# Kernel optimization log

Hardware: AMD Instinct MI355X
Metric: run time of the kernel (lower is better)

The kernel has to match this reference:

```python
import jax, jax.numpy as jnp
import numpy as np


def setup_inputs() -> dict:
    key = jax.random.key(0)
    kq, kk, kv = jax.random.split(key, 3)
    B, S, D = 8, 2048, 128
    Q = jax.random.normal(kq, (B, S, D), dtype=jnp.float32)
    K = jax.random.normal(kk, (B, S, D), dtype=jnp.float32)
    V = jax.random.normal(kv, (B, S, D), dtype=jnp.float32)
    return {"Q": Q, "K": K, "V": V}


def reference(Q, K, V):
    # scores: [B, S, S]
    d = Q.shape[-1]
    scores = jnp.einsum('bqd,bkd->bqk', Q, K) / jnp.sqrt(jnp.float32(d))
    # causal mask: position i attends to keys <= i (original sets upper triangle to -inf)
    S = scores.shape[-1]
    causal = jnp.tril(jnp.ones((S, S), dtype=bool))  # [S, S]
    scores = jnp.where(causal[None, :, :], scores, -jnp.inf)
    probs = jax.nn.softmax(scores, axis=-1)
    return jnp.einsum('bqk,bkd->bqd', probs, V)
```

## Files before the change

### kernel.cpp

```cpp
#include <hip/hip_runtime.h>

#define BB 8
#define SS 2048
#define DD 128

typedef _Float16 f16;
typedef _Float16 f16x8 __attribute__((ext_vector_type(8)));
typedef float f32x4 __attribute__((ext_vector_type(4)));

#define SWV(d) ((((d) & 7) ^ (((d) >> 3) & 7)) << 3)

static __device__ __forceinline__ unsigned short f2h(float x) {
    f16 h = (f16)x;
    return __builtin_bit_cast(unsigned short, h);
}

static __device__ __forceinline__ float fast_exp2(float x) {
#if __has_builtin(__builtin_amdgcn_exp2f)
    return __builtin_amdgcn_exp2f(x);
#else
    return exp2f(x);
#endif
}

template <int NS>
__global__ __launch_bounds__(256, 2)
void attn_fwd(const float* __restrict__ Qg, const float* __restrict__ Kg,
              const float* __restrict__ Vg, float* __restrict__ Og,
              float* __restrict__ Opart, float2* __restrict__ mlb)
{
    __shared__ __align__(16) f16 Kl[64 * 128];
    __shared__ __align__(16) f16 Vt[128 * 64];
    __shared__ __align__(16) f16 Pl[4][16 * 64];

    const int tid  = threadIdx.x;
    const int lane = tid & 63;
    const int w    = tid >> 6;
    const int c_   = lane & 15;
    const int g    = lane >> 4;

    const int L   = blockIdx.x;
    const int bb  = L & 7;
    const int rem = L >> 3;
    const int qb  = 31 - (rem / NS);
    const int s   = rem % NS;
    const int T   = qb + 1;
    const int t0  = (T * s) / NS;
    const int t1  = (T * (s + 1)) / NS;

    const int qrow0 = qb * 64 + w * 16;

    const float qs = 0.08838834764831845f * 1.4426950408889634f;
    f16x8 qf[4];
    {
        const float* qp = Qg + (size_t)(bb * SS + qrow0 + c_) * DD;
#pragma unroll
        for (int kk = 0; kk < 4; ++kk) {
            const int d0 = kk * 32 + g * 8;
            f32x4 a = *(const f32x4*)(qp + d0);
            f32x4 b = *(const f32x4*)(qp + d0 + 4);
            f16x8 q;
#pragma unroll
            for (int i = 0; i < 4; ++i) {
                q[i]     = (f16)(a[i] * qs);
                q[i + 4] = (f16)(b[i] * qs);
            }
            qf[kk] = q;
        }
    }

    f32x4 Oa[8];
#pragma unroll
    for (int i = 0; i < 8; ++i) Oa[i] = (f32x4){0.f, 0.f, 0.f, 0.f};
    float mrun[4] = {-1e30f, -1e30f, -1e30f, -1e30f};
    float lpart[4] = {0.f, 0.f, 0.f, 0.f};

    f16* Pw = &Pl[w][0];

    const int krow = tid >> 5;
    const int kc4  = tid & 31;
    const int vkg  = tid >> 5;
    const int vq   = tid & 31;

    f32x4 kreg[8], vreg[8];

    if (t0 < t1) {
        {
            const size_t gb = (size_t)(bb * SS + t0 * 64) * DD;
#pragma unroll
            for (int j = 0; j < 8; ++j)
                kreg[j] = *(const f32x4*)(Kg + gb + (krow + 8 * j) * DD + kc4 * 4);
#pragma unroll
            for (int i = 0; i < 8; ++i)
                vreg[i] = *(const f32x4*)(Vg + gb + (vkg * 8 + i) * DD + vq * 4);
        }

        for (int t = t0; t < t1; ++t) {
            __syncthreads();
#pragma unroll
            for (int j = 0; j < 8; ++j) {
                const int row = krow + 8 * j;
                const int el  = row * 128 + ((kc4 * 4) ^ ((row & 7) << 3));
                f32x4 v = kreg[j];
                ushort4 u;
                u.x = f2h(v[0]); u.y = f2h(v[1]); u.z = f2h(v[2]); u.w = f2h(v[3]);
                *(ushort4*)&Kl[el] = u;
            }
#pragma unroll
            for (int dd = 0; dd < 4; ++dd) {
                const int d  = vq * 4 + dd;
                const int sw = SWV(d);
#pragma unroll
                for (int h = 0; h < 2; ++h) {
                    ushort4 u;
                    u.x = f2h(vreg[4 * h + 0][dd]);
                    u.y = f2h(vreg[4 * h + 1][dd]);
                    u.z = f2h(vreg[4 * h + 2][dd]);
                    u.w = f2h(vreg[4 * h + 3][dd]);
                    const int el = d * 64 + ((vkg * 8 + 4 * h) ^ sw);
                    *(ushort4*)&Vt[el] = u;
                }
            }
            __syncthreads();

            if (t + 1 < t1) {
                const size_t gb = (size_t)(bb * SS + (t + 1) * 64) * DD;
#pragma unroll
                for (int j = 0; j < 8; ++j)
                    kreg[j] = *(const f32x4*)(Kg + gb + (krow + 8 * j) * DD + kc4 * 4);
#pragma unroll
                for (int i = 0; i < 8; ++i)
                    vreg[i] = *(const f32x4*)(Vg + gb + (vkg * 8 + i) * DD + vq * 4);
            }

            const int kbase = t * 64;

            f32x4 s4[4];
            __builtin_amdgcn_s_setprio(1);
#pragma unroll
            for (int nb = 0; nb < 4; ++nb) {
                f32x4 acc = (f32x4){0.f, 0.f, 0.f, 0.f};
                const int row = c_ + nb * 16;
                const int sw  = (row & 7) << 3;
#pragma unroll
                for (int kk = 0; kk < 4; ++kk) {
                    f16x8 kb = *(const f16x8*)&Kl[row * 128 + ((kk * 32 + g * 8) ^ sw)];
                    acc = __builtin_amdgcn_mfma_f32_16x16x32_f16(qf[kk], kb, acc, 0, 0, 0);
                }
                s4[nb] = acc;
            }
            __builtin_amdgcn_s_setprio(0);

            if (t == qb) {
#pragma unroll
                for (int nb = 0; nb < 4; ++nb)
#pragma unroll
                    for (int r = 0; r < 4; ++r) {
                        const int kj = kbase + nb * 16 + c_;
                        const int qi = qrow0 + g * 4 + r;
                        if (kj > qi) s4[nb][r] = -1e30f;
                    }
            }

            float pm[4], sc[4];
#pragma unroll
            for (int r = 0; r < 4; ++r) {
                float v = fmaxf(fmaxf(s4[0][r], s4[1][r]), fmaxf(s4[2][r], s4[3][r]));
                v = fmaxf(v, __shfl_xor(v, 1));
                v = fmaxf(v, __shfl_xor(v, 2));
                v = fmaxf(v, __shfl_xor(v, 4));
                v = fmaxf(v, __shfl_xor(v, 8));
                pm[r] = v;
            }
#pragma unroll
            for (int r = 0; r < 4; ++r) {
                const bool keep = (pm[r] - mrun[r] <= 8.0f);
                const float mn  = keep ? mrun[r] : pm[r];
                sc[r]   = keep ? 1.0f : fast_exp2(mrun[r] - pm[r]);
                mrun[r] = mn;
            }
            float rs[4] = {0.f, 0.f, 0.f, 0.f};
            f16 pv16[4][4];
#pragma unroll
            for (int nb = 0; nb < 4; ++nb)
#pragma unroll
                for (int r = 0; r < 4; ++r) {
                    float pv = fast_exp2(s4[nb][r] - mrun[r]);
                    rs[r] += pv;
                    pv16[nb][r] = (f16)pv;
                }
            const float scmin = fminf(fminf(sc[0], sc[1]), fminf(sc[2], sc[3]));
            if (scmin < 1.0f) {
#pragma unroll
                for (int dblk = 0; dblk < 8; ++dblk)
#pragma unroll
                    for (int r = 0; r < 4; ++r) Oa[dblk][r] *= sc[r];
            }
#pragma unroll
            for (int r = 0; r < 4; ++r) lpart[r] = lpart[r] * sc[r] + rs[r];

#pragma unroll
            for (int nb = 0; nb < 4; ++nb)
#pragma unroll
                for (int r = 0; r < 4; ++r) {
                    const int row = g * 4 + r;
                    Pw[row * 64 + ((nb * 16 + c_) ^ ((row & 7) << 3))] = pv16[nb][r];
                }

#pragma unroll
            for (int ks = 0; ks < 2; ++ks) {
                f16x8 pa = *(const f16x8*)&Pw[c_ * 64 + ((ks * 32 + g * 8) ^ ((c_ & 7) << 3))];
                __builtin_amdgcn_s_setprio(1);
#pragma unroll
                for (int dblk = 0; dblk < 8; ++dblk) {
                    const int d  = dblk * 16 + c_;
                    f16x8 vb = *(const f16x8*)&Vt[d * 64 + ((ks * 32 + g * 8) ^ SWV(d))];
                    Oa[dblk] = __builtin_amdgcn_mfma_f32_16x16x32_f16(pa, vb, Oa[dblk], 0, 0, 0);
                }
                __builtin_amdgcn_s_setprio(0);
            }
        }
    }

    float lrun[4];
#pragma unroll
    for (int r = 0; r < 4; ++r) {
        float v = lpart[r];
        v += __shfl_xor(v, 1);
        v += __shfl_xor(v, 2);
        v += __shfl_xor(v, 4);
        v += __shfl_xor(v, 8);
        lrun[r] = v;
    }

    if (NS == 1) {
#pragma unroll
        for (int r = 0; r < 4; ++r) {
            const int qrow = qrow0 + g * 4 + r;
            float* dst = Og + (size_t)(bb * SS + qrow) * DD + c_;
            const float inv = 1.0f / lrun[r];
#pragma unroll
            for (int dblk = 0; dblk < 8; ++dblk) dst[dblk * 16] = Oa[dblk][r] * inv;
        }
    } else {
        float*  od  = (s == 0) ? Og : (Opart + (size_t)(s - 1) * BB * SS * DD);
        float2* mld = mlb + (size_t)s * BB * SS;
#pragma unroll
        for (int r = 0; r < 4; ++r) {
            const int qrow = qrow0 + g * 4 + r;
            float* dst = od + (size_t)(bb * SS + qrow) * DD + c_;
#pragma unroll
            for (int dblk = 0; dblk < 8; ++dblk) dst[dblk * 16] = Oa[dblk][r];
            if (c_ == 0) mld[bb * SS + qrow] = make_float2(mrun[r], lrun[r]);
        }
    }
}

template <int NS>
__global__ __launch_bounds__(256)
void merge_kernel(float* __restrict__ out, const float* __restrict__ Opart,
                  const float2* __restrict__ mlb)
{
    const int idx = blockIdx.x * 256 + threadIdx.x;
    const int row = idx >> 5;
    float2 ml[NS];
#pragma unroll
    for (int i = 0; i < NS; ++i) ml[i] = mlb[(size_t)i * BB * SS + row];
    float mm = ml[0].x;
#pragma unroll
    for (int i = 1; i < NS; ++i) mm = fmaxf(mm, ml[i].x);
    float e[NS], den = 0.f;
#pragma unroll
    for (int i = 0; i < NS; ++i) {
        e[i] = fast_exp2(ml[i].x - mm);
        den += ml[i].y * e[i];
    }
    const float inv = 1.0f / den;
    float4 o = ((const float4*)out)[idx];
    float4 acc;
    acc.x = o.x * e[0]; acc.y = o.y * e[0];
    acc.z = o.z * e[0]; acc.w = o.w * e[0];
#pragma unroll
    for (int i = 1; i < NS; ++i) {
        float4 p = ((const float4*)(Opart + (size_t)(i - 1) * BB * SS * DD))[idx];
        acc.x += p.x * e[i]; acc.y += p.y * e[i];
        acc.z += p.z * e[i]; acc.w += p.w * e[i];
    }
    acc.x *= inv; acc.y *= inv; acc.z *= inv; acc.w *= inv;
    ((float4*)out)[idx] = acc;
}

extern "C" void kernel_launch(void* const* d_in, const int* in_sizes, int n_in,
                              void* d_out, int out_size, void* d_ws, size_t ws_size,
                              hipStream_t stream)
{
    const float* Q = (const float*)d_in[0];
    const float* K = (const float*)d_in[1];
    const float* V = (const float*)d_in[2];
    float* out = (float*)d_out;

    const size_t OB = (size_t)BB * SS * DD * sizeof(float);
    const size_t MB_ = (size_t)BB * SS * sizeof(float2);
    const int mergeGrid = BB * SS * DD / 4 / 256;

    const size_t need4 = 3 * OB + 4 * MB_;
    const size_t need2 = 1 * OB + 2 * MB_;

    if (ws_size >= need4) {
        float*  Op  = (float*)d_ws;
        float2* mlb = (float2*)((char*)d_ws + 3 * OB);
        hipLaunchKernelGGL((attn_fwd<4>), dim3(8 * 32 * 4), dim3(256), 0, stream,
                           Q, K, V, out, Op, mlb);
        hipLaunchKernelGGL((merge_kernel<4>), dim3(mergeGrid), dim3(256), 0, stream,
                           out, Op, mlb);
    } else if (ws_size >= need2) {
        float*  Op  = (float*)d_ws;
        float2* mlb = (float2*)((char*)d_ws + 1 * OB);
        hipLaunchKernelGGL((attn_fwd<2>), dim3(8 * 32 * 2), dim3(256), 0, stream,
                           Q, K, V, out, Op, mlb);
        hipLaunchKernelGGL((merge_kernel<2>), dim3(mergeGrid), dim3(256), 0, stream,
                           out, Op, mlb);
    } else {
        hipLaunchKernelGGL((attn_fwd<1>), dim3(8 * 32), dim3(256), 0, stream,
                           Q, K, V, out, (float*)nullptr, (float2*)nullptr);
    }
}
```

Baseline: 105.7 us.

## Store split partials in fp16, raise split count to 8, warp-level deferred rescale

Partial outputs from the split-K attention blocks are now written as fp16 to a workspace for every split, including split 0, and the merge kernel reads eight halves per thread. This halves partial-output traffic and allows an 8-way split when the workspace is large enough. The online softmax now checks the max with a single wave-wide reduction and skips the per-row rescale when all rows stay within a threshold of 4. Conversions to fp16 use packed cvt_pkrtz. The risks are reduced precision in the partials and more merge work at 8 splits.

```diff
diff --git a/kernel.cpp b/kernel.cpp
--- a/kernel.cpp
+++ b/kernel.cpp
@@ -3,17 +3,17 @@
 #define BB 8
 #define SS 2048
 #define DD 128
+#define SEG ((size_t)BB * SS * DD)
 
 typedef _Float16 f16;
+typedef _Float16 f16x2 __attribute__((ext_vector_type(2)));
+typedef __fp16 h16x2 __attribute__((ext_vector_type(2)));
 typedef _Float16 f16x8 __attribute__((ext_vector_type(8)));
 typedef float f32x4 __attribute__((ext_vector_type(4)));
 
 #define SWV(d) ((((d) & 7) ^ (((d) >> 3) & 7)) << 3)
 
-static __device__ __forceinline__ unsigned short f2h(float x) {
-    f16 h = (f16)x;
-    return __builtin_bit_cast(unsigned short, h);
-}
+#define DEFER_THR 4.0f
 
 static __device__ __forceinline__ float fast_exp2(float x) {
 #if __has_builtin(__builtin_amdgcn_exp2f)
@@ -23,11 +23,25 @@
 #endif
 }
 
+static __device__ __forceinline__ f16x2 cvt_pk(float a, float b) {
+    h16x2 r = __builtin_amdgcn_cvt_pkrtz(a, b);
+    return __builtin_bit_cast(f16x2, r);
+}
+
+static __device__ __forceinline__ uint2 pack4(f32x4 v) {
+    f16x2 lo = cvt_pk(v[0], v[1]);
+    f16x2 hi = cvt_pk(v[2], v[3]);
+    uint2 u;
+    u.x = __builtin_bit_cast(unsigned int, lo);
+    u.y = __builtin_bit_cast(unsigned int, hi);
+    return u;
+}
+
 template <int NS>
 __global__ __launch_bounds__(256, 2)
 void attn_fwd(const float* __restrict__ Qg, const float* __restrict__ Kg,
               const float* __restrict__ Vg, float* __restrict__ Og,
-              float* __restrict__ Opart, float2* __restrict__ mlb)
+              f16* __restrict__ Opf, float2* __restrict__ mlb)
 {
     __shared__ __align__(16) f16 Kl[64 * 128];
     __shared__ __align__(16) f16 Vt[128 * 64];
@@ -43,10 +57,10 @@
     const int bb  = L & 7;
     const int rem = L >> 3;
     const int qb  = 31 - (rem / NS);
-    const int s   = rem % NS;
+    const int sg  = rem % NS;
     const int T   = qb + 1;
-    const int t0  = (T * s) / NS;
-    const int t1  = (T * (s + 1)) / NS;
+    const int t0  = (T * sg) / NS;
+    const int t1  = (T * (sg + 1)) / NS;
 
     const int qrow0 = qb * 64 + w * 16;
 
@@ -101,10 +115,7 @@
             for (int j = 0; j < 8; ++j) {
                 const int row = krow + 8 * j;
                 const int el  = row * 128 + ((kc4 * 4) ^ ((row & 7) << 3));
-                f32x4 v = kreg[j];
-                ushort4 u;
-                u.x = f2h(v[0]); u.y = f2h(v[1]); u.z = f2h(v[2]); u.w = f2h(v[3]);
-                *(ushort4*)&Kl[el] = u;
+                *(uint2*)&Kl[el] = pack4(kreg[j]);
             }
 #pragma unroll
             for (int dd = 0; dd < 4; ++dd) {
@@ -112,13 +123,10 @@
                 const int sw = SWV(d);
 #pragma unroll
                 for (int h = 0; h < 2; ++h) {
-                    ushort4 u;
-                    u.x = f2h(vreg[4 * h + 0][dd]);
-                    u.y = f2h(vreg[4 * h + 1][dd]);
-                    u.z = f2h(vreg[4 * h + 2][dd]);
-                    u.w = f2h(vreg[4 * h + 3][dd]);
+                    f32x4 vv = {vreg[4 * h + 0][dd], vreg[4 * h + 1][dd],
+                                vreg[4 * h + 2][dd], vreg[4 * h + 3][dd]};
                     const int el = d * 64 + ((vkg * 8 + 4 * h) ^ sw);
-                    *(ushort4*)&Vt[el] = u;
+                    *(uint2*)&Vt[el] = pack4(vv);
                 }
             }
             __syncthreads();
@@ -162,50 +170,64 @@
                     }
             }
 
-            float pm[4], sc[4];
-#pragma unroll
-            for (int r = 0; r < 4; ++r) {
-                float v = fmaxf(fmaxf(s4[0][r], s4[1][r]), fmaxf(s4[2][r], s4[3][r]));
-                v = fmaxf(v, __shfl_xor(v, 1));
-                v = fmaxf(v, __shfl_xor(v, 2));
-                v = fmaxf(v, __shfl_xor(v, 4));
-                v = fmaxf(v, __shfl_xor(v, 8));
-                pm[r] = v;
-            }
-#pragma unroll
-            for (int r = 0; r < 4; ++r) {
-                const bool keep = (pm[r] - mrun[r] <= 8.0f);
-                const float mn  = keep ? mrun[r] : pm[r];
-                sc[r]   = keep ? 1.0f : fast_exp2(mrun[r] - pm[r]);
-                mrun[r] = mn;
-            }
-            float rs[4] = {0.f, 0.f, 0.f, 0.f};
-            f16 pv16[4][4];
-#pragma unroll
-            for (int nb = 0; nb < 4; ++nb)
+            float wm = -1e30f;
+#pragma unroll
+            for (int nb = 0; nb < 4; ++nb) {
+                f32x4 v = s4[nb];
+                wm = fmaxf(wm, fmaxf(fmaxf(v[0], v[1]), fmaxf(v[2], v[3])));
+            }
+            wm = fmaxf(wm, __shfl_xor(wm, 1));
+            wm = fmaxf(wm, __shfl_xor(wm, 2));
+            wm = fmaxf(wm, __shfl_xor(wm, 4));
+            wm = fmaxf(wm, __shfl_xor(wm, 8));
+            wm = fmaxf(wm, __shfl_xor(wm, 16));
+            wm = fmaxf(wm, __shfl_xor(wm, 32));
+            float mrmin = fminf(fminf(mrun[0], mrun[1]), fminf(mrun[2], mrun[3]));
+
+            if (!__all(wm - mrmin <= DEFER_THR)) {
+                float sc[4];
+                float scmin = 1.0f;
 #pragma unroll
                 for (int r = 0; r < 4; ++r) {
-                    float pv = fast_exp2(s4[nb][r] - mrun[r]);
-                    rs[r] += pv;
-                    pv16[nb][r] = (f16)pv;
-                }
-            const float scmin = fminf(fminf(sc[0], sc[1]), fminf(sc[2], sc[3]));
-            if (scmin < 1.0f) {
-#pragma unroll
-                for (int dblk = 0; dblk < 8; ++dblk)
-#pragma unroll
-                    for (int r = 0; r < 4; ++r) Oa[dblk][r] *= sc[r];
-            }
-#pragma unroll
-            for (int r = 0; r < 4; ++r) lpart[r] = lpart[r] * sc[r] + rs[r];
-
-#pragma unroll
-            for (int nb = 0; nb < 4; ++nb)
+                    float pm = fmaxf(fmaxf(s4[0][r], s4[1][r]),
+                                     fmaxf(s4[2][r], s4[3][r]));
+                    pm = fmaxf(pm, __shfl_xor(pm, 1));
+                    pm = fmaxf(pm, __shfl_xor(pm, 2));
+                    pm = fmaxf(pm, __shfl_xor(pm, 4));
+                    pm = fmaxf(pm, __shfl_xor(pm, 8));
+                    const bool keep = (pm - mrun[r] <= DEFER_THR);
+                    sc[r] = keep ? 1.0f : fast_exp2(mrun[r] - pm);
+                    if (!keep) mrun[r] = pm;
+                    scmin = fminf(scmin, sc[r]);
+                }
+                if (scmin < 1.0f) {
+#pragma unroll
+                    for (int r = 0; r < 4; ++r) {
+                        lpart[r] *= sc[r];
+#pragma unroll
+                        for (int dblk = 0; dblk < 8; ++dblk)
+                            Oa[dblk][r] *= sc[r];
+                    }
+                }
+            }
+
+#pragma unroll
+            for (int nb = 0; nb < 4; ++nb) {
+                float pv[4];
+#pragma unroll
+                for (int r = 0; r < 4; ++r) {
+                    pv[r] = fast_exp2(s4[nb][r] - mrun[r]);
+                    lpart[r] += pv[r];
+                }
+                f16x2 p01 = cvt_pk(pv[0], pv[1]);
+                f16x2 p23 = cvt_pk(pv[2], pv[3]);
 #pragma unroll
                 for (int r = 0; r < 4; ++r) {
                     const int row = g * 4 + r;
-                    Pw[row * 64 + ((nb * 16 + c_) ^ ((row & 7) << 3))] = pv16[nb][r];
-                }
+                    const f16 hv = (r < 2) ? p01[r & 1] : p23[r & 1];
+                    Pw[row * 64 + ((nb * 16 + c_) ^ ((row & 7) << 3))] = hv;
+                }
+            }
 
 #pragma unroll
             for (int ks = 0; ks < 2; ++ks) {
@@ -240,17 +262,19 @@
             float* dst = Og + (size_t)(bb * SS + qrow) * DD + c_;
             const float inv = 1.0f / lrun[r];
 #pragma unroll
-            for (int dblk = 0; dblk < 8; ++dblk) dst[dblk * 16] = Oa[dblk][r] * inv;
+            for (int dblk = 0; dblk < 8; ++dblk)
+                dst[dblk * 16] = Oa[dblk][r] * inv;
         }
     } else {
-        float*  od  = (s == 0) ? Og : (Opart + (size_t)(s - 1) * BB * SS * DD);
-        float2* mld = mlb + (size_t)s * BB * SS;
+        f16*    od  = Opf + (size_t)sg * SEG;
+        float2* mld = mlb + (size_t)sg * BB * SS;
 #pragma unroll
         for (int r = 0; r < 4; ++r) {
             const int qrow = qrow0 + g * 4 + r;
-            float* dst = od + (size_t)(bb * SS + qrow) * DD + c_;
-#pragma unroll
-            for (int dblk = 0; dblk < 8; ++dblk) dst[dblk * 16] = Oa[dblk][r];
+            f16* dst = od + (size_t)(bb * SS + qrow) * DD + c_;
+#pragma unroll
+            for (int dblk = 0; dblk < 8; ++dblk)
+                dst[dblk * 16] = (f16)Oa[dblk][r];
             if (c_ == 0) mld[bb * SS + qrow] = make_float2(mrun[r], lrun[r]);
         }
     }
@@ -258,11 +282,11 @@
 
 template <int NS>
 __global__ __launch_bounds__(256)
-void merge_kernel(float* __restrict__ out, const float* __restrict__ Opart,
+void merge_kernel(float* __restrict__ out, const f16* __restrict__ Opf,
                   const float2* __restrict__ mlb)
 {
     const int idx = blockIdx.x * 256 + threadIdx.x;
-    const int row = idx >> 5;
+    const int row = idx >> 4;
     float2 ml[NS];
 #pragma unroll
     for (int i = 0; i < NS; ++i) ml[i] = mlb[(size_t)i * BB * SS + row];
@@ -276,18 +300,20 @@
         den += ml[i].y * e[i];
     }
     const float inv = 1.0f / den;
-    float4 o = ((const float4*)out)[idx];
-    float4 acc;
-    acc.x = o.x * e[0]; acc.y = o.y * e[0];
-    acc.z = o.z * e[0]; acc.w = o.w * e[0];
-#pragma unroll
-    for (int i = 1; i < NS; ++i) {
-        float4 p = ((const float4*)(Opart + (size_t)(i - 1) * BB * SS * DD))[idx];
-        acc.x += p.x * e[i]; acc.y += p.y * e[i];
-        acc.z += p.z * e[i]; acc.w += p.w * e[i];
-    }
-    acc.x *= inv; acc.y *= inv; acc.z *= inv; acc.w *= inv;
-    ((float4*)out)[idx] = acc;
+
+    float acc[8] = {0.f, 0.f, 0.f, 0.f, 0.f, 0.f, 0.f, 0.f};
+#pragma unroll
+    for (int i = 0; i < NS; ++i) {
+        f16x8 v = *(const f16x8*)(Opf + (size_t)i * SEG + (size_t)idx * 8);
+#pragma unroll
+        for (int j = 0; j < 8; ++j) acc[j] += (float)v[j] * e[i];
+    }
+    float4 o0, o1;
+    o0.x = acc[0] * inv; o0.y = acc[1] * inv; o0.z = acc[2] * inv; o0.w = acc[3] * inv;
+    o1.x = acc[4] * inv; o1.y = acc[5] * inv; o1.z = acc[6] * inv; o1.w = acc[7] * inv;
+    float4* dst = (float4*)(out + (size_t)idx * 8);
+    dst[0] = o0;
+    dst[1] = o1;
 }
 
 extern "C" void kernel_launch(void* const* d_in, const int* in_sizes, int n_in,
@@ -299,29 +325,29 @@
     const float* V = (const float*)d_in[2];
     float* out = (float*)d_out;
 
-    const size_t OB = (size_t)BB * SS * DD * sizeof(float);
-    const size_t MB_ = (size_t)BB * SS * sizeof(float2);
-    const int mergeGrid = BB * SS * DD / 4 / 256;
-
-    const size_t need4 = 3 * OB + 4 * MB_;
-    const size_t need2 = 1 * OB + 2 * MB_;
-
-    if (ws_size >= need4) {
-        float*  Op  = (float*)d_ws;
-        float2* mlb = (float2*)((char*)d_ws + 3 * OB);
+    const size_t OPB = SEG * sizeof(f16);
+    const size_t MLB = (size_t)BB * SS * sizeof(float2);
+    const int mergeGrid = (int)(SEG / 8 / 256);
+
+    const size_t need8 = 8 * OPB + 8 * MLB;
+    const size_t need4 = 4 * OPB + 4 * MLB;
+
+    if (ws_size >= need8) {
+        f16*    Opf = (f16*)d_ws;
+        float2* mlb = (float2*)((char*)d_ws + 8 * OPB);
+        hipLaunchKernelGGL((attn_fwd<8>), dim3(8 * 32 * 8), dim3(256), 0, stream,
+                           Q, K, V, out, Opf, mlb);
+        hipLaunchKernelGGL((merge_kernel<8>), dim3(mergeGrid), dim3(256), 0, stream,
+                           out, Opf, mlb);
+    } else if (ws_size >= need4) {
+        f16*    Opf = (f16*)d_ws;
+        float2* mlb = (float2*)((char*)d_ws + 4 * OPB);
         hipLaunchKernelGGL((attn_fwd<4>), dim3(8 * 32 * 4), dim3(256), 0, stream,
-                           Q, K, V, out, Op, mlb);
+                           Q, K, V, out, Opf, mlb);
         hipLaunchKernelGGL((merge_kernel<4>), dim3(mergeGrid), dim3(256), 0, stream,
-                           out, Op, mlb);
-    } else if (ws_size >= need2) {
-        float*  Op  = (float*)d_ws;
-        float2* mlb = (float2*)((char*)d_ws + 1 * OB);
-        hipLaunchKernelGGL((attn_fwd<2>), dim3(8 * 32 * 2), dim3(256), 0, stream,
-                           Q, K, V, out, Op, mlb);
-        hipLaunchKernelGGL((merge_kernel<2>), dim3(mergeGrid), dim3(256), 0, stream,
-                           out, Op, mlb);
+                           out, Opf, mlb);
     } else {
         hipLaunchKernelGGL((attn_fwd<1>), dim3(8 * 32), dim3(256), 0, stream,
-                           Q, K, V, out, (float*)nullptr, (float2*)nullptr);
-    }
-}
+                           Q, K, V, out, (f16*)nullptr, (float2*)nullptr);
+    }
+}
```

Result: slower. 113.8 us (+7.7%).
